# Kernel optimization log

Measured on AMD Instinct MI355X. Metric: run time of the kernel, lower is better.

Reference implementation:

```python
import jax, jax.numpy as jnp
import numpy as np

D_MODEL = 1024
N_HEADS = 16
HEAD_DIM = D_MODEL // N_HEADS


def setup_inputs() -> dict:
    key = jax.random.key(0)
    ks = jax.random.split(key, 10)
    B, NQ, S = 8, 64, 4096
    inv = 1.0 / np.sqrt(D_MODEL)
    inp = {
        "queries": jax.random.normal(ks[0], (B, NQ, D_MODEL), dtype=jnp.float32),
        "context": jax.random.normal(ks[1], (B, S, D_MODEL), dtype=jnp.float32),
        "wq": jax.random.normal(ks[2], (D_MODEL, D_MODEL), dtype=jnp.float32) * inv,
        "bq": jnp.zeros((D_MODEL,), dtype=jnp.float32),
        "wk": jax.random.normal(ks[3], (D_MODEL, D_MODEL), dtype=jnp.float32) * inv,
        "bk": jnp.zeros((D_MODEL,), dtype=jnp.float32),
        "wv": jax.random.normal(ks[4], (D_MODEL, D_MODEL), dtype=jnp.float32) * inv,
        "bv": jnp.zeros((D_MODEL,), dtype=jnp.float32),
        "wo": jax.random.normal(ks[5], (D_MODEL, D_MODEL), dtype=jnp.float32) * inv,
        "bo": jnp.zeros((D_MODEL,), dtype=jnp.float32),
    }
    return inp


def reference(queries, context, wq, bq, wk, bk, wv, bv, wo, bo):
    B, NQ, D = queries.shape
    S = context.shape[1]
    H, HD = N_HEADS, HEAD_DIM
    scale = HD ** -0.5
    # projections (x @ W^T + b, matching nn.Linear)
    q = queries @ wq.T + bq            # (B, NQ, D)
    k = context @ wk.T + bk            # (B, S, D)
    v = context @ wv.T + bv            # (B, S, D)
    q = q.reshape(B, NQ, H, HD).transpose(0, 2, 1, 3)  # (B, H, NQ, HD)
    k = k.reshape(B, S, H, HD).transpose(0, 2, 1, 3)   # (B, H, S, HD)
    v = v.reshape(B, S, H, HD).transpose(0, 2, 1, 3)   # (B, H, S, HD)
    attn = jnp.einsum('bhnd,bhsd->bhns', q, k) * scale
    attn = jax.nn.softmax(attn, axis=-1)
    # dropout is identity at eval / p=0
    out = jnp.einsum('bhns,bhsd->bhnd', attn, v)        # (B, H, NQ, HD)
    out = out.transpose(0, 2, 1, 3).reshape(B, NQ, D)   # (B, NQ, D)
    return out @ wo.T + bo
```

## Files before the change

kernel.cpp:

```cpp
#include <hip/hip_runtime.h>
#include <stdint.h>

#define BATCH   8
#define NQL     64
#define SLEN    4096
#define DMODEL  1024
#define NHEADS  16
#define HDIM    64
#define NSPLIT  8

typedef float          f32x4  __attribute__((ext_vector_type(4)));
typedef float          f32x16 __attribute__((ext_vector_type(16)));
typedef __bf16         bf16x8 __attribute__((ext_vector_type(8)));
typedef unsigned int   u32x4  __attribute__((ext_vector_type(4)));
typedef unsigned short u16x4  __attribute__((ext_vector_type(4)));
typedef unsigned short u16x8  __attribute__((ext_vector_type(8)));

__device__ __forceinline__ unsigned short f2bf(float f) {
  unsigned int u = __builtin_bit_cast(unsigned int, f);
  u += 0x7FFFu + ((u >> 16) & 1u);
  return (unsigned short)(u >> 16);
}

__device__ __forceinline__ f32x4 mfma16(bf16x8 a, bf16x8 b, f32x4 c) {
  return __builtin_amdgcn_mfma_f32_16x16x32_bf16(a, b, c, 0, 0, 0);
}

__device__ __forceinline__ bf16x8 lds_frag(const char* p) {
  u32x4 v = *(const u32x4*)p;
  return __builtin_bit_cast(bf16x8, v);
}

__device__ __forceinline__ void gload_lds16(const void* g, void* l) {
  __builtin_amdgcn_global_load_lds((const __attribute__((address_space(1))) void*)g,
                                   (__attribute__((address_space(3))) void*)l, 16, 0, 0);
}

__global__ __launch_bounds__(256) void cvt_bf16_kernel(const float* __restrict__ in,
                                                       unsigned short* __restrict__ out,
                                                       int n8) {
  int i = blockIdx.x * 256 + threadIdx.x;
  if (i >= n8) return;
  const float4* p = (const float4*)in + (size_t)i * 2;
  float4 a = p[0], b = p[1];
  u16x8 o;
  o[0] = f2bf(a.x); o[1] = f2bf(a.y); o[2] = f2bf(a.z); o[3] = f2bf(a.w);
  o[4] = f2bf(b.x); o[5] = f2bf(b.y); o[6] = f2bf(b.z); o[7] = f2bf(b.w);
  *((u16x8*)out + i) = o;
}

#define GF32(a) ((a) ^ ((((a) >> 7) & 3) << 4))

template<int MODE>
__global__ __launch_bounds__(512, 2)
void gemm256(const unsigned short* __restrict__ A, const unsigned short* __restrict__ Bw,
             const float* __restrict__ bias, void* __restrict__ Cout,
             int M, int N, int K) {
  __shared__ char lds[131072];

  const int tid = threadIdx.x;
  const int wid = tid >> 6, lane = tid & 63;
  const int l31 = lane & 31, lhi = lane >> 5;
  const int wm = wid >> 2, wn = wid & 3;

  const int nbn = N >> 8;
  const int cpx = (int)gridDim.x >> 3;
  const int bid = (int)blockIdx.x;
  const int wg  = (bid & 7) * cpx + (bid >> 3);
  const int brow = (wg / nbn) << 8;
  const int bcol = (wg % nbn) << 8;

  const int aswz = GF32(tid * 16);
  const int srow = aswz >> 6;
  const int skoe = (aswz & 63) >> 1;
  const unsigned short* sA0 = A  + (size_t)(brow + srow) * K + skoe;
  const unsigned short* sA1 = A  + (size_t)(brow + 128 + srow) * K + skoe;
  const unsigned short* sB0 = Bw + (size_t)(bcol + srow) * K + skoe;
  const unsigned short* sB1 = Bw + (size_t)(bcol + 128 + srow) * K + skoe;
  const int dd = wid * 1024;

  int offA[4][2], offB[2][2];
#pragma unroll
  for (int mi = 0; mi < 4; ++mi)
#pragma unroll
    for (int ks = 0; ks < 2; ++ks) {
      int r = wm * 128 + mi * 32 + l31;
      int a = r * 64 + ks * 32 + lhi * 16;
      offA[mi][ks] = GF32(a);
    }
#pragma unroll
  for (int ni = 0; ni < 2; ++ni)
#pragma unroll
    for (int ks = 0; ks < 2; ++ks) {
      int r = wn * 64 + ni * 32 + l31;
      int a = r * 64 + ks * 32 + lhi * 16;
      offB[ni][ks] = 16384 + GF32(a);
    }

  f32x16 acc[4][2];
#pragma unroll
  for (int mi = 0; mi < 4; ++mi)
#pragma unroll
    for (int ni = 0; ni < 2; ++ni)
#pragma unroll
      for (int e = 0; e < 16; ++e) acc[mi][ni][e] = 0.f;

  auto stageA = [&](int kt, int slot) {
    const int ko = kt << 5;
    char* sb = lds + (slot << 15);
    gload_lds16(sA0 + ko, sb + dd);
    gload_lds16(sA1 + ko, sb + 8192 + dd);
  };
  auto stageB = [&](int kt, int slot) {
    const int ko = kt << 5;
    char* sb = lds + (slot << 15) + 16384;
    gload_lds16(sB0 + ko, sb + dd);
    gload_lds16(sB1 + ko, sb + 8192 + dd);
  };

  const int KT = K >> 5;
  stageA(0, 0); stageB(0, 0);
  stageA(1, 1); stageB(1, 1);
  stageA(2, 2); stageB(2, 2);
  asm volatile("s_waitcnt vmcnt(8)" ::: "memory");
  __builtin_amdgcn_s_barrier();
  __builtin_amdgcn_sched_barrier(0);

  for (int kt = 0; kt < KT; ++kt) {
    const char* cur = lds + ((kt & 3) << 15);
    const int pf = kt + 3;
    const int ps = pf & 3;

    {
      bf16x8 af[4], bf[2];
#pragma unroll
      for (int mi = 0; mi < 4; ++mi) af[mi] = lds_frag(cur + offA[mi][0]);
#pragma unroll
      for (int ni = 0; ni < 2; ++ni) bf[ni] = lds_frag(cur + offB[ni][0]);
      if (pf < KT) stageA(pf, ps);
      __builtin_amdgcn_s_barrier();
      asm volatile("s_waitcnt lgkmcnt(0)" ::: "memory");
      __builtin_amdgcn_sched_barrier(0);
      __builtin_amdgcn_s_setprio(1);
#pragma unroll
      for (int mi = 0; mi < 4; ++mi)
#pragma unroll
        for (int ni = 0; ni < 2; ++ni)
          acc[mi][ni] = __builtin_amdgcn_mfma_f32_32x32x16_bf16(af[mi], bf[ni],
                                                                acc[mi][ni], 0, 0, 0);
      __builtin_amdgcn_s_setprio(0);
      __builtin_amdgcn_sched_barrier(0);
      __builtin_amdgcn_s_barrier();
      __builtin_amdgcn_sched_barrier(0);
    }
    {
      bf16x8 af[4], bf[2];
#pragma unroll
      for (int mi = 0; mi < 4; ++mi) af[mi] = lds_frag(cur + offA[mi][1]);
#pragma unroll
      for (int ni = 0; ni < 2; ++ni) bf[ni] = lds_frag(cur + offB[ni][1]);
      if (pf < KT) stageB(pf, ps);
      asm volatile("s_waitcnt vmcnt(8)" ::: "memory");
      __builtin_amdgcn_s_barrier();
      asm volatile("s_waitcnt lgkmcnt(0)" ::: "memory");
      __builtin_amdgcn_sched_barrier(0);
      __builtin_amdgcn_s_setprio(1);
#pragma unroll
      for (int mi = 0; mi < 4; ++mi)
#pragma unroll
        for (int ni = 0; ni < 2; ++ni)
          acc[mi][ni] = __builtin_amdgcn_mfma_f32_32x32x16_bf16(af[mi], bf[ni],
                                                                acc[mi][ni], 0, 0, 0);
      __builtin_amdgcn_s_setprio(0);
      __builtin_amdgcn_sched_barrier(0);
      __builtin_amdgcn_s_barrier();
      __builtin_amdgcn_sched_barrier(0);
    }
  }

#pragma unroll
  for (int mi = 0; mi < 4; ++mi) {
#pragma unroll
    for (int ni = 0; ni < 2; ++ni) {
      f32x16 v = acc[mi][ni];
      const int c = bcol + wn * 64 + ni * 32 + l31;
      const float bi = bias[c];
      const int rbase = brow + wm * 128 + mi * 32 + lhi * 4;
      if constexpr (MODE == 0) {
        unsigned short* Cb = (unsigned short*)Cout;
#pragma unroll
        for (int q = 0; q < 4; ++q)
#pragma unroll
          for (int j = 0; j < 4; ++j)
            Cb[(size_t)(rbase + q * 8 + j) * N + c] = f2bf(v[q * 4 + j] + bi);
      } else {
        unsigned short* Vt = (unsigned short*)Cout;
        const size_t fb = ((size_t)(rbase >> 12) * 1024 + c) * 4096;
#pragma unroll
        for (int q = 0; q < 4; ++q) {
          u16x4 pk;
#pragma unroll
          for (int j = 0; j < 4; ++j) pk[j] = f2bf(v[q * 4 + j] + bi);
          *(u16x4*)(Vt + fb + ((rbase + q * 8) & 4095)) = pk;
        }
      }
    }
  }
}

template<int MODE>
__global__ __launch_bounds__(256)
void gemm_bt(const unsigned short* __restrict__ A, const unsigned short* __restrict__ Bw,
             const float* __restrict__ bias, void* __restrict__ Cout,
             int M, int N, int K) {
  __shared__ char lds[65536];

  const int tid  = threadIdx.x;
  const int wave = tid >> 6, lane = tid & 63;
  const int g    = lane >> 4, ln = lane & 15;
  const int nbn  = N >> 7;
  const int brow = (int)(blockIdx.x / nbn) << 7;
  const int bcol = (int)(blockIdx.x % nbn) << 7;
  const int wr   = wave >> 1, wc = wave & 1;

  f32x4 acc[4][4];
#pragma unroll
  for (int i = 0; i < 4; ++i)
#pragma unroll
    for (int j = 0; j < 4; ++j) acc[i][j] = (f32x4){0.f, 0.f, 0.f, 0.f};

  const int KT = K >> 6;
  const int srow = lane >> 3;
  const int srcs = (lane & 7) ^ (srow & 7);

  auto stage = [&](int kt, char* buf) {
#pragma unroll
    for (int c = wave; c < 16; c += 4) {
      int row = (c << 3) + srow;
      const char* ga = (const char*)A + (((size_t)(brow + row) * K + (kt << 6) + (srcs << 3)) << 1);
      gload_lds16(ga, buf + (c << 10));
      const char* gb = (const char*)Bw + (((size_t)(bcol + row) * K + (kt << 6) + (srcs << 3)) << 1);
      gload_lds16(gb, buf + 16384 + (c << 10));
    }
  };

  stage(0, lds);
  for (int kt = 0; kt < KT; ++kt) {
    char* cur = lds + ((kt & 1) << 15);
    if (kt + 1 < KT) {
      stage(kt + 1, lds + (((kt + 1) & 1) << 15));
      asm volatile("s_waitcnt vmcnt(8)" ::: "memory");
    } else {
      asm volatile("s_waitcnt vmcnt(0)" ::: "memory");
    }
    __builtin_amdgcn_s_barrier();
    __builtin_amdgcn_sched_barrier(0);

#pragma unroll
    for (int ks = 0; ks < 2; ++ks) {
      bf16x8 af[4], bfr[4];
      const int slot = ((ks << 2) + g) ^ (ln & 7);
#pragma unroll
      for (int mt = 0; mt < 4; ++mt) {
        int row = wr * 64 + mt * 16 + ln;
        af[mt] = lds_frag(cur + row * 128 + (slot << 4));
      }
#pragma unroll
      for (int nt = 0; nt < 4; ++nt) {
        int row = wc * 64 + nt * 16 + ln;
        bfr[nt] = lds_frag(cur + 16384 + row * 128 + (slot << 4));
      }
      __builtin_amdgcn_s_setprio(1);
#pragma unroll
      for (int mt = 0; mt < 4; ++mt)
#pragma unroll
        for (int nt = 0; nt < 4; ++nt)
          acc[mt][nt] = mfma16(af[mt], bfr[nt], acc[mt][nt]);
      __builtin_amdgcn_s_setprio(0);
    }
    __builtin_amdgcn_s_barrier();
  }

#pragma unroll
  for (int mt = 0; mt < 4; ++mt) {
#pragma unroll
    for (int nt = 0; nt < 4; ++nt) {
      f32x4 v = acc[mt][nt];
      int r0 = brow + wr * 64 + mt * 16 + g * 4;
      int c  = bcol + wc * 64 + nt * 16 + ln;
      float bi = bias[c];
      if constexpr (MODE == 0) {
        unsigned short* Cb = (unsigned short*)Cout;
#pragma unroll
        for (int j = 0; j < 4; ++j) Cb[(size_t)(r0 + j) * N + c] = f2bf(v[j] + bi);
      } else {
        float* Cf = (float*)Cout;
#pragma unroll
        for (int j = 0; j < 4; ++j) Cf[(size_t)(r0 + j) * N + c] = v[j] + bi;
      }
    }
  }
}

__global__ __launch_bounds__(256)
void attn_split(const unsigned short* __restrict__ Qp,
                const unsigned short* __restrict__ Kp,
                const unsigned short* __restrict__ Vt,
                float* __restrict__ Opart,
                float* __restrict__ Mpart,
                float* __restrict__ Lpart) {
  __shared__ char ldsKV[2][16384];
  __shared__ unsigned int plds[4 * 16 * 36];

  const int bh = (int)blockIdx.x / NSPLIT;
  const int sp = (int)blockIdx.x % NSPLIT;
  const int b = bh >> 4, h = bh & 15;
  const int tid = threadIdx.x;
  const int wave = tid >> 6, lane = tid & 63;
  const int g = lane >> 4, ln = lane & 15;
  const int pbase = wave * 576 + ln * 36;
  const int srow = lane >> 3;
  const int srcs = (lane & 7) ^ (srow & 7);

  const unsigned short* qb =
      Qp + ((size_t)(b * 64 + wave * 16 + ln) * 1024) + h * 64 + g * 8;
  bf16x8 qf[2];
  qf[0] = __builtin_bit_cast(bf16x8, *(const u32x4*)qb);
  qf[1] = __builtin_bit_cast(bf16x8, *(const u32x4*)(qb + 32));

  f32x4 oacc[4];
#pragma unroll
  for (int i = 0; i < 4; ++i) oacc[i] = (f32x4){0.f, 0.f, 0.f, 0.f};
  float mrun = -1e30f, lrun = 0.f;

  auto stage = [&](int t, int buf) {
    int s0 = t << 6;
    char* bK = ldsKV[buf];
#pragma unroll
    for (int c4 = 0; c4 < 4; ++c4) {
      int c = wave * 4 + c4;
      int cc = c & 7;
      int row = (cc << 3) + srow;
      const char* gsrc;
      if (c < 8)
        gsrc = (const char*)Kp + (((size_t)((b << 12) + s0 + row) * 1024 + (h << 6) + (srcs << 3)) << 1);
      else
        gsrc = (const char*)Vt + (((size_t)((b << 10) + (h << 6) + row) * 4096 + s0 + (srcs << 3)) << 1);
      gload_lds16(gsrc, bK + ((c < 8) ? 0 : 8192) + (cc << 10));
    }
  };

  const int T0 = sp * (SLEN / 64 / NSPLIT);
  const int NTL = SLEN / 64 / NSPLIT;
  stage(T0, 0);
  for (int tl = 0; tl < NTL; ++tl) {
    asm volatile("s_waitcnt vmcnt(0)" ::: "memory");
    __syncthreads();
    if (tl + 1 < NTL) stage(T0 + tl + 1, (tl + 1) & 1);

    char* bufK = ldsKV[tl & 1];
    char* bufV = bufK + 8192;

    f32x4 s4[4];
#pragma unroll
    for (int i = 0; i < 4; ++i) s4[i] = (f32x4){0.f, 0.f, 0.f, 0.f};
    __builtin_amdgcn_s_setprio(1);
#pragma unroll
    for (int ks = 0; ks < 2; ++ks) {
      const int slot = ((ks << 2) + g) ^ (ln & 7);
#pragma unroll
      for (int mt = 0; mt < 4; ++mt) {
        int row = mt * 16 + ln;
        s4[mt] = mfma16(lds_frag(bufK + row * 128 + (slot << 4)), qf[ks], s4[mt]);
      }
    }
    __builtin_amdgcn_s_setprio(0);

    float tmax = -1e30f;
#pragma unroll
    for (int mt = 0; mt < 4; ++mt)
#pragma unroll
      for (int j = 0; j < 4; ++j) {
        float sv = s4[mt][j] * 0.125f;
        s4[mt][j] = sv;
        tmax = fmaxf(tmax, sv);
      }
    tmax = fmaxf(tmax, __shfl_xor(tmax, 16));
    tmax = fmaxf(tmax, __shfl_xor(tmax, 32));
    float mnew = fmaxf(mrun, tmax);
    float factor = __expf(mrun - mnew);
    float psum = 0.f;
#pragma unroll
    for (int mt = 0; mt < 4; ++mt) {
      float p0 = __expf(s4[mt][0] - mnew);
      float p1 = __expf(s4[mt][1] - mnew);
      float p2 = __expf(s4[mt][2] - mnew);
      float p3 = __expf(s4[mt][3] - mnew);
      psum += (p0 + p1) + (p2 + p3);
      plds[pbase + mt * 8 + g * 2 + 0] = (unsigned)f2bf(p0) | ((unsigned)f2bf(p1) << 16);
      plds[pbase + mt * 8 + g * 2 + 1] = (unsigned)f2bf(p2) | ((unsigned)f2bf(p3) << 16);
    }
    psum += __shfl_xor(psum, 16);
    psum += __shfl_xor(psum, 32);
    lrun = lrun * factor + psum;
    mrun = mnew;

    float fj0 = __shfl(factor, g * 4 + 0);
    float fj1 = __shfl(factor, g * 4 + 1);
    float fj2 = __shfl(factor, g * 4 + 2);
    float fj3 = __shfl(factor, g * 4 + 3);
#pragma unroll
    for (int nt = 0; nt < 4; ++nt) {
      oacc[nt][0] *= fj0; oacc[nt][1] *= fj1; oacc[nt][2] *= fj2; oacc[nt][3] *= fj3;
    }

    __builtin_amdgcn_s_setprio(1);
#pragma unroll
    for (int kt2 = 0; kt2 < 2; ++kt2) {
      u32x4 pv;
      int pidx = pbase + kt2 * 16 + g * 4;
      pv[0] = plds[pidx]; pv[1] = plds[pidx + 1]; pv[2] = plds[pidx + 2]; pv[3] = plds[pidx + 3];
      bf16x8 pa = __builtin_bit_cast(bf16x8, pv);
      const int slot = ((kt2 << 2) + g) ^ (ln & 7);
#pragma unroll
      for (int nt = 0; nt < 4; ++nt) {
        int row = nt * 16 + ln;
        oacc[nt] = mfma16(pa, lds_frag(bufV + row * 128 + (slot << 4)), oacc[nt]);
      }
    }
    __builtin_amdgcn_s_setprio(0);
  }

  const int rowb = sp * (BATCH * NHEADS * 64) + bh * 64;
#pragma unroll
  for (int nt = 0; nt < 4; ++nt) {
#pragma unroll
    for (int j = 0; j < 4; ++j) {
      int q = wave * 16 + g * 4 + j;
      Opart[(size_t)(rowb + q) * 64 + nt * 16 + ln] = oacc[nt][j];
    }
  }
  if (g == 0) {
    Mpart[rowb + wave * 16 + ln] = mrun;
    Lpart[rowb + wave * 16 + ln] = lrun;
  }
}

__global__ __launch_bounds__(256)
void attn_combine(const float* __restrict__ Opart, const float* __restrict__ Mpart,
                  const float* __restrict__ Lpart, unsigned short* __restrict__ Aout) {
  const int blk = blockIdx.x;
  const int bh = blk >> 4;
  const int q  = ((blk & 15) << 2) + (threadIdx.x >> 6);
  const int hd = threadIdx.x & 63;
  const int row = bh * 64 + q;

  float mi[NSPLIT];
  float M = -1e30f;
#pragma unroll
  for (int i = 0; i < NSPLIT; ++i) {
    mi[i] = Mpart[i * 8192 + row];
    M = fmaxf(M, mi[i]);
  }
  float L = 0.f, o = 0.f;
#pragma unroll
  for (int i = 0; i < NSPLIT; ++i) {
    float w = __expf(mi[i] - M);
    L += Lpart[i * 8192 + row] * w;
    o += Opart[(size_t)(i * 8192 + row) * 64 + hd] * w;
  }
  const int b = bh >> 4, h = bh & 15;
  Aout[(size_t)(b * 64 + q) * 1024 + h * 64 + hd] = f2bf(o / L);
}

extern "C" void kernel_launch(void* const* d_in, const int* in_sizes, int n_in,
                              void* d_out, int out_size, void* d_ws, size_t ws_size,
                              hipStream_t stream) {
  const float* queries = (const float*)d_in[0];
  const float* context = (const float*)d_in[1];
  const float* wq = (const float*)d_in[2];
  const float* bq = (const float*)d_in[3];
  const float* wk = (const float*)d_in[4];
  const float* bk = (const float*)d_in[5];
  const float* wv = (const float*)d_in[6];
  const float* bv = (const float*)d_in[7];
  const float* wo = (const float*)d_in[8];
  const float* bo = (const float*)d_in[9];

  const size_t CTX_E = (size_t)BATCH * SLEN * DMODEL;
  const size_t QRY_E = (size_t)BATCH * NQL * DMODEL;
  const size_t W_E   = (size_t)DMODEL * DMODEL;

  char* ws = (char*)d_ws;
  size_t off = 0;
  auto alloc = [&](size_t bytes) {
    char* p = ws + off;
    off += (bytes + 255) & ~(size_t)255;
    return p;
  };
  unsigned short* ctx_bf = (unsigned short*)alloc(CTX_E * 2);
  unsigned short* q_bf   = (unsigned short*)alloc(QRY_E * 2);
  unsigned short* wq_bf  = (unsigned short*)alloc(W_E * 2);
  unsigned short* wk_bf  = (unsigned short*)alloc(W_E * 2);
  unsigned short* wv_bf  = (unsigned short*)alloc(W_E * 2);
  unsigned short* wo_bf  = (unsigned short*)alloc(W_E * 2);
  unsigned short* Qp     = (unsigned short*)alloc(QRY_E * 2);
  unsigned short* Kp     = (unsigned short*)alloc(CTX_E * 2);
  unsigned short* Vt     = (unsigned short*)alloc(CTX_E * 2);
  unsigned short* Ao     = (unsigned short*)alloc(QRY_E * 2);
  if (off > ws_size) return;

  float* Opart = (float*)ctx_bf;
  float* Mpart = Opart + (size_t)NSPLIT * BATCH * NHEADS * 64 * 64;
  float* Lpart = Mpart + (size_t)NSPLIT * BATCH * NHEADS * 64;

  cvt_bf16_kernel<<<dim3((int)(CTX_E / 8 / 256)), 256, 0, stream>>>(context, ctx_bf, (int)(CTX_E / 8));
  cvt_bf16_kernel<<<dim3((int)(QRY_E / 8 / 256)), 256, 0, stream>>>(queries, q_bf, (int)(QRY_E / 8));
  cvt_bf16_kernel<<<dim3((int)(W_E / 8 / 256)), 256, 0, stream>>>(wq, wq_bf, (int)(W_E / 8));
  cvt_bf16_kernel<<<dim3((int)(W_E / 8 / 256)), 256, 0, stream>>>(wk, wk_bf, (int)(W_E / 8));
  cvt_bf16_kernel<<<dim3((int)(W_E / 8 / 256)), 256, 0, stream>>>(wv, wv_bf, (int)(W_E / 8));
  cvt_bf16_kernel<<<dim3((int)(W_E / 8 / 256)), 256, 0, stream>>>(wo, wo_bf, (int)(W_E / 8));

  const int M_KV = BATCH * SLEN;
  const int M_Q  = BATCH * NQL;

  gemm256<0><<<dim3((M_KV / 256) * (DMODEL / 256)), 512, 0, stream>>>(ctx_bf, wk_bf, bk, Kp, M_KV, DMODEL, DMODEL);
  gemm256<2><<<dim3((M_KV / 256) * (DMODEL / 256)), 512, 0, stream>>>(ctx_bf, wv_bf, bv, Vt, M_KV, DMODEL, DMODEL);

  gemm_bt<0><<<dim3((M_Q / 128) * (DMODEL / 128)), 256, 0, stream>>>(q_bf, wq_bf, bq, Qp, M_Q, DMODEL, DMODEL);

  attn_split<<<dim3(BATCH * NHEADS * NSPLIT), 256, 0, stream>>>(Qp, Kp, Vt, Opart, Mpart, Lpart);
  attn_combine<<<dim3(BATCH * NHEADS * 16), 256, 0, stream>>>(Opart, Mpart, Lpart, Ao);

  gemm_bt<1><<<dim3((M_Q / 128) * (DMODEL / 128)), 256, 0, stream>>>(Ao, wo_bf, bo, d_out, M_Q, DMODEL, DMODEL);
}
```

Before: 457.4 us.

## Double-buffer LDS fragments in GEMM mainloop to overlap reads with MFMA

Restructures the projection GEMM mainloop so the register fragments for the next half-step are read from LDS while the current half-step's MFMAs run, using two register fragment sets (af0/bf0, af1/bf1). This replaces the per-half 'load, wait lgkmcnt(0), compute' pattern and removes the explicit LDS waits. The vmcnt waits are retuned for the tail iterations and the number of barriers per iteration drops. It adds register pressure from the extra fragment set and depends on the compiler inserting correct LDS waits before each use.

```diff
diff --git a/kernel.cpp b/kernel.cpp
--- a/kernel.cpp
+++ b/kernel.cpp
@@ -126,56 +126,54 @@
   __builtin_amdgcn_s_barrier();
   __builtin_amdgcn_sched_barrier(0);
 
+  bf16x8 af0[4], bf0[2], af1[4], bf1[2];
+#pragma unroll
+  for (int mi = 0; mi < 4; ++mi) af0[mi] = lds_frag(lds + offA[mi][0]);
+#pragma unroll
+  for (int ni = 0; ni < 2; ++ni) bf0[ni] = lds_frag(lds + offB[ni][0]);
+
   for (int kt = 0; kt < KT; ++kt) {
     const char* cur = lds + ((kt & 3) << 15);
+    const char* nxt = lds + (((kt + 1) & 3) << 15);
     const int pf = kt + 3;
     const int ps = pf & 3;
 
-    {
-      bf16x8 af[4], bf[2];
-#pragma unroll
-      for (int mi = 0; mi < 4; ++mi) af[mi] = lds_frag(cur + offA[mi][0]);
-#pragma unroll
-      for (int ni = 0; ni < 2; ++ni) bf[ni] = lds_frag(cur + offB[ni][0]);
-      if (pf < KT) stageA(pf, ps);
-      __builtin_amdgcn_s_barrier();
-      asm volatile("s_waitcnt lgkmcnt(0)" ::: "memory");
-      __builtin_amdgcn_sched_barrier(0);
-      __builtin_amdgcn_s_setprio(1);
-#pragma unroll
-      for (int mi = 0; mi < 4; ++mi)
-#pragma unroll
-        for (int ni = 0; ni < 2; ++ni)
-          acc[mi][ni] = __builtin_amdgcn_mfma_f32_32x32x16_bf16(af[mi], bf[ni],
-                                                                acc[mi][ni], 0, 0, 0);
-      __builtin_amdgcn_s_setprio(0);
-      __builtin_amdgcn_sched_barrier(0);
-      __builtin_amdgcn_s_barrier();
-      __builtin_amdgcn_sched_barrier(0);
-    }
-    {
-      bf16x8 af[4], bf[2];
-#pragma unroll
-      for (int mi = 0; mi < 4; ++mi) af[mi] = lds_frag(cur + offA[mi][1]);
-#pragma unroll
-      for (int ni = 0; ni < 2; ++ni) bf[ni] = lds_frag(cur + offB[ni][1]);
-      if (pf < KT) stageB(pf, ps);
-      asm volatile("s_waitcnt vmcnt(8)" ::: "memory");
-      __builtin_amdgcn_s_barrier();
-      asm volatile("s_waitcnt lgkmcnt(0)" ::: "memory");
-      __builtin_amdgcn_sched_barrier(0);
-      __builtin_amdgcn_s_setprio(1);
-#pragma unroll
-      for (int mi = 0; mi < 4; ++mi)
-#pragma unroll
-        for (int ni = 0; ni < 2; ++ni)
-          acc[mi][ni] = __builtin_amdgcn_mfma_f32_32x32x16_bf16(af[mi], bf[ni],
-                                                                acc[mi][ni], 0, 0, 0);
-      __builtin_amdgcn_s_setprio(0);
-      __builtin_amdgcn_sched_barrier(0);
-      __builtin_amdgcn_s_barrier();
-      __builtin_amdgcn_sched_barrier(0);
-    }
+#pragma unroll
+    for (int mi = 0; mi < 4; ++mi) af1[mi] = lds_frag(cur + offA[mi][1]);
+#pragma unroll
+    for (int ni = 0; ni < 2; ++ni) bf1[ni] = lds_frag(cur + offB[ni][1]);
+    if (pf < KT) stageA(pf, ps);
+    __builtin_amdgcn_s_setprio(1);
+#pragma unroll
+    for (int mi = 0; mi < 4; ++mi)
+#pragma unroll
+      for (int ni = 0; ni < 2; ++ni)
+        acc[mi][ni] = __builtin_amdgcn_mfma_f32_32x32x16_bf16(af0[mi], bf0[ni],
+                                                              acc[mi][ni], 0, 0, 0);
+    __builtin_amdgcn_s_setprio(0);
+    if (kt < KT - 3)       asm volatile("s_waitcnt vmcnt(6)" ::: "memory");
+    else if (kt == KT - 3) asm volatile("s_waitcnt vmcnt(4)" ::: "memory");
+    else                   asm volatile("s_waitcnt vmcnt(0)" ::: "memory");
+    __builtin_amdgcn_s_barrier();
+    __builtin_amdgcn_sched_barrier(0);
+
+    if (kt + 1 < KT) {
+#pragma unroll
+      for (int mi = 0; mi < 4; ++mi) af0[mi] = lds_frag(nxt + offA[mi][0]);
+#pragma unroll
+      for (int ni = 0; ni < 2; ++ni) bf0[ni] = lds_frag(nxt + offB[ni][0]);
+    }
+    if (pf < KT) stageB(pf, ps);
+    __builtin_amdgcn_s_setprio(1);
+#pragma unroll
+    for (int mi = 0; mi < 4; ++mi)
+#pragma unroll
+      for (int ni = 0; ni < 2; ++ni)
+        acc[mi][ni] = __builtin_amdgcn_mfma_f32_32x32x16_bf16(af1[mi], bf1[ni],
+                                                              acc[mi][ni], 0, 0, 0);
+    __builtin_amdgcn_s_setprio(0);
+    __builtin_amdgcn_s_barrier();
+    __builtin_amdgcn_sched_barrier(0);
   }
 
 #pragma unroll
```

Measured after the change: 458.2 us. No clear change (+0.2%).
